# Performance work log

Hardware: AMD Instinct MI355X
Metric: run time of the kernel (lower is better)

Reference implementation:

```python
import jax, jax.numpy as jnp
import numpy as np

B, T, N, F_IN = 8, 12, 10000, 1
H = 32          # hidden_size
K = 2           # gnn_kernel (diffusion steps)
HORIZON = 12
E = 320000      # n_nodes * avg_degree 32


def setup_inputs() -> dict:
    key = jax.random.key(0)
    ks = jax.random.split(key, 12)
    s = 0.1  # weight scale to keep GRU in sane range
    return {
        "x": jax.random.normal(ks[0], (B, T, N, F_IN), jnp.float32),
        "edge_index": jax.random.randint(ks[1], (2, E), 0, N, dtype=jnp.int64),
        "edge_weight": jax.random.uniform(ks[2], (E,), jnp.float32),
        "enc_w": jax.random.normal(ks[3], (F_IN, H), jnp.float32) * s,
        "enc_b": jnp.zeros((H,), jnp.float32),
        "node_emb": jax.random.normal(ks[4], (N, H), jnp.float32) * s,
        "w_ih": jax.random.normal(ks[5], (3 * H, H), jnp.float32) * s,
        "w_hh": jax.random.normal(ks[6], (3 * H, H), jnp.float32) * s,
        "b_ih": jnp.zeros((3 * H,), jnp.float32),
        "b_hh": jnp.zeros((3 * H,), jnp.float32),
        "filt_w": jax.random.normal(ks[7], ((2 * K + 1) * H, H), jnp.float32) * s,
        "filt_b": jnp.zeros((H,), jnp.float32),
        "dec_w": jax.random.normal(ks[8], (H, F_IN * HORIZON), jnp.float32) * s,
        "dec_b": jnp.zeros((F_IN * HORIZON,), jnp.float32),
    }


def _gru_last(xs, w_ih, w_hh, b_ih, b_hh):
    # xs: [t, bn, H] -> last hidden state [bn, H]
    t, bn, h = xs.shape
    gx = jnp.einsum('tbh,gh->tbg', xs, w_ih) + b_ih  # [t, bn, 3H]

    def step(hid, gx_t):
        gh = hid @ w_hh.T + b_hh
        xr, xz, xn = jnp.split(gx_t, 3, axis=-1)
        hr, hz, hn = jnp.split(gh, 3, axis=-1)
        r = jax.nn.sigmoid(xr + hr)
        z = jax.nn.sigmoid(xz + hz)
        n_ = jnp.tanh(xn + r * hn)
        hid = (1.0 - z) * n_ + z * hid
        return hid, None

    h0 = jnp.zeros((bn, h), xs.dtype)
    h_last, _ = jax.lax.scan(step, h0, gx)
    return h_last


def _propagate(x, src, tgt, w, n):
    # x: [b, n, H]; out[:, tgt] += w * x[:, src]
    msgs = x[:, src, :] * w[None, :, None]  # [b, E, H]
    return jnp.zeros_like(x).at[:, tgt, :].add(msgs)


def reference(x, edge_index, edge_weight, enc_w, enc_b, node_emb,
              w_ih, w_hh, b_ih, b_hh, filt_w, filt_b, dec_w, dec_b):
    b, t, n, f_in = x.shape
    h = enc_w.shape[1]

    # ---- encoder + node embeddings ----
    x_enc = x @ enc_w + enc_b                       # [b, t, n, H]
    x_emb = x_enc + node_emb[None, None]            # broadcast add

    # ---- temporal GRU (per node, batch_first, last state) ----
    xs = jnp.transpose(x_emb, (1, 0, 2, 3)).reshape(t, b * n, h)
    h_time = _gru_last(xs, w_ih, w_hh, b_ih, b_hh).reshape(b, n, h)

    # ---- DiffConv: k-hop forward + backward diffusion ----
    src, tgt = edge_index[0], edge_index[1]
    deg_f = jnp.zeros((n,), edge_weight.dtype).at[tgt].add(edge_weight)
    w_f = edge_weight / jnp.where(deg_f[tgt] > 0, deg_f[tgt], 1.0)
    deg_b = jnp.zeros((n,), edge_weight.dtype).at[src].add(edge_weight)
    w_b = edge_weight / jnp.where(deg_b[src] > 0, deg_b[src], 1.0)

    outs = [h_time]  # root weight
    x_sup = h_time
    for _ in range(K):  # forward transition hops
        x_sup = _propagate(x_sup, src, tgt, w_f, n)
        outs.append(x_sup)
    x_sup = h_time
    for _ in range(K):  # backward (reversed edges) hops
        x_sup = _propagate(x_sup, tgt, src, w_b, n)
        outs.append(x_sup)
    z = jnp.concatenate(outs, axis=-1) @ filt_w + filt_b  # [b, n, H]

    # ---- decoder + rearrange 'b n (t f) -> b t n f' ----
    out = z @ dec_w + dec_b                                # [b, n, horizon*f_in]
    out = out.reshape(b, n, HORIZON, f_in)
    return jnp.transpose(out, (0, 2, 1, 3))                # [b, horizon, n, f_in]
```

## Files before the change

### kernel.cpp

```cpp
#include <hip/hip_runtime.h>
#include <hip/hip_fp16.h>

#define BB 8
#define TT 12
#define NN 10000
#define HH 32
#define EE 320000
#define HOR 12
#define NCB 157

static __device__ __forceinline__ float sigm(float x) {
    return __builtin_amdgcn_rcpf(1.0f + __expf(-x));
}
static __device__ __forceinline__ float tanh_fast(float x) {
    return 1.0f - 2.0f * __builtin_amdgcn_rcpf(1.0f + __expf(2.0f * x));
}
static __device__ __forceinline__ float2 uph2(unsigned u) {
    __half2 h = *(__half2*)&u;
    return __half22float2(h);
}
static __device__ __forceinline__ unsigned pkh2(float a, float b) {
    __half2 h = __floats2half2_rn(a, b);
    return *(unsigned*)&h;
}

typedef _Float16 f16x4 __attribute__((ext_vector_type(4)));
typedef float    f32x4 __attribute__((ext_vector_type(4)));

__global__ void k_zero(uint4* __restrict__ p, int n4) {
    int i = blockIdx.x * blockDim.x + threadIdx.x;
    if (i < n4) p[i] = (uint4){0u, 0u, 0u, 0u};
}

__global__ void k_cbhist(const float* __restrict__ node_emb, const float* __restrict__ enc_b,
                     const float* __restrict__ w_ih, const float* __restrict__ b_ih,
                     const float* __restrict__ b_hh,
                     const float* __restrict__ enc_w, const float* __restrict__ filt_w,
                     const float* __restrict__ filt_b, const float* __restrict__ dec_w,
                     const float* __restrict__ dec_b,
                     float* __restrict__ CB, float* __restrict__ A,
                     float* __restrict__ W2, float* __restrict__ b2,
                     const int* __restrict__ ei,
                     int* cnt_f, int* cnt_b,
                     int* __restrict__ rank_f, int* __restrict__ rank_b) {
    __shared__ float sw[96*36];
    __shared__ float semb[64*36];
    __shared__ float sbias[96];
    int bid = blockIdx.x;
    int tid = threadIdx.x;
    if (bid < NCB) {
        int n0 = bid * 64;
        for (int i = tid; i < 96*32; i += 256) {
            int g = i >> 5, h = i & 31;
            sw[g*36 + h] = w_ih[i];
        }
        for (int i = tid; i < 64*32; i += 256) {
            int row = i >> 5, h = i & 31;
            int n = n0 + row; if (n >= NN) n = NN-1;
            semb[row*36 + h] = enc_b[h] + node_emb[(size_t)n*32 + h];
        }
        if (tid < 96) sbias[tid] = b_ih[tid] + (tid < 64 ? b_hh[tid] : 0.f);
        __syncthreads();
        #pragma unroll 1
        for (int i = 0; i < 24; i++) {
            int o = i*256 + tid;
            int row = o / 96, g = o - row*96;
            int n = n0 + row;
            if (n < NN) {
                float s = sbias[g];
                const float4* ev = (const float4*)(semb + row*36);
                const float4* wv = (const float4*)(sw + g*36);
                #pragma unroll
                for (int q = 0; q < 8; q++) {
                    float4 e = ev[q], w = wv[q];
                    s = fmaf(e.x, w.x, s); s = fmaf(e.y, w.y, s);
                    s = fmaf(e.z, w.z, s); s = fmaf(e.w, w.w, s);
                }
                CB[(size_t)n*96 + g] = s;
            }
        }
    } else if (bid == NCB) {
        for (int i = tid; i < 96 + 160*12 + 12; i += blockDim.x) {
            if (i < 96) {
                float s = 0.f;
                for (int h = 0; h < HH; h++) s += enc_w[h] * w_ih[i*HH + h];
                A[i] = s;
            } else if (i < 96 + 1920) {
                int j = i - 96; int c = j / 12, o = j % 12;
                float s = 0.f;
                for (int h = 0; h < HH; h++) s += filt_w[c*HH + h] * dec_w[h*12 + o];
                W2[j] = s;
            } else {
                int o = i - 2016;
                float s = dec_b[o];
                for (int h = 0; h < HH; h++) s += filt_b[h] * dec_w[h*12 + o];
                b2[o] = s;
            }
        }
    } else {
        int e = (bid - NCB - 1) * 256 + tid;
        int s = ei[e], t = ei[EE + e];
        rank_f[e] = atomicAdd(&cnt_f[t], 1);
        rank_b[e] = atomicAdd(&cnt_b[s], 1);
    }
}

__global__ void k_scan(const int* __restrict__ cnt_f, int* off_f,
                       const int* __restrict__ cnt_b, int* off_b) {
    const int* cnt; int* off;
    if (blockIdx.x == 0) { cnt = cnt_f; off = off_f; }
    else                 { cnt = cnt_b; off = off_b; }
    __shared__ int part[1024];
    int t = threadIdx.x;
    const int CH = (NN + 1023) / 1024;
    int beg = t * CH, end = min(beg + CH, NN);
    int s = 0;
    for (int i = beg; i < end; i++) s += cnt[i];
    part[t] = s;
    __syncthreads();
    for (int d = 1; d < 1024; d <<= 1) {
        int add = (t >= d) ? part[t - d] : 0;
        __syncthreads();
        part[t] += add;
        __syncthreads();
    }
    int run = part[t] - s;
    for (int i = beg; i < end; i++) {
        off[i] = run; run += cnt[i];
    }
    if (t == 1023) off[NN] = part[1023];
}

__global__ __launch_bounds__(256) void k_grufill(const float* __restrict__ x,
                      const float* __restrict__ CB, const float* __restrict__ Ag,
                      const float* __restrict__ w_hh, const float* __restrict__ b_hh,
                      __half* __restrict__ hout16,
                      const int* __restrict__ ei, const float* __restrict__ ew,
                      const int* __restrict__ off_f, const int* __restrict__ rank_f,
                      unsigned long long* __restrict__ cfe,
                      const int* __restrict__ off_b, const int* __restrict__ rank_b,
                      unsigned long long* __restrict__ cbe) {
    int tid = threadIdx.x;
    if (blockIdx.x >= 1250) {
        int e = (blockIdx.x - 1250) * 256 + tid;
        int s = ei[e], t = ei[EE + e]; float w = ew[e];
        unsigned long long wb = (unsigned long long)__float_as_uint(w) << 32;
        cfe[off_f[t] + rank_f[e]] = wb | (unsigned)s;
        cbe[off_b[s] + rank_b[e]] = wb | (unsigned)t;
        return;
    }
    __shared__ unsigned sW[1536];
    __shared__ __half  shh[4][16*40];
    __shared__ float   sx[64][12];
    int r0b = blockIdx.x * 64;

    for (int d = tid; d < 1536; d += 256) {
        int fi = d >> 1, epair = d & 1;
        int l = fi & 63, tk = fi >> 6;
        int gt = tk >> 1, kh = tk & 1;
        int gate = 16*gt + (l & 15);
        int k = kh*16 + ((l >> 4) << 2) + 2*epair;
        sW[d] = pkh2(w_hh[gate*32 + k], w_hh[gate*32 + k + 1]);
    }
    for (int i = tid; i < 64*12; i += 256) {
        int row = i / 12, t = i - row*12;
        int r = r0b + row; int b = r / NN, n = r - b*NN;
        sx[row][t] = x[((size_t)b*TT + t)*NN + n];
    }
    __syncthreads();

    const int wv = tid >> 6, l = tid & 63;
    const int c = l & 15, m = l >> 4;
    const int r0w = r0b + wv*16;

    int bb[4], nn_[4];
    #pragma unroll
    for (int q = 0; q < 4; q++) {
        int r = r0w + 4*m + q;
        bb[q] = r / NN; nn_[q] = r - bb[q]*NN;
    }

    float cNx[2][4];
    f32x4 crv[2], czv[2], cnv[2];
    float aRj[2], aZj[2], aNj[2], bn0c[2];
    #pragma unroll
    for (int t2 = 0; t2 < 2; t2++) {
        int j = 16*t2 + c;
        #pragma unroll
        for (int q = 0; q < 4; q++) {
            const float* cb = CB + (size_t)nn_[q]*96;
            crv[t2][q] = cb[j];
            czv[t2][q] = cb[32 + j];
            cNx[t2][q] = cb[64 + j];
        }
        bn0c[t2] = b_hh[64 + j];
        cnv[t2] = (f32x4){bn0c[t2], bn0c[t2], bn0c[t2], bn0c[t2]};
        aRj[t2] = Ag[j]; aZj[t2] = Ag[32 + j]; aNj[t2] = Ag[64 + j];
    }

    f16x4 bf[12];
    #pragma unroll
    for (int i = 0; i < 12; i++) {
        unsigned long long v = *(const unsigned long long*)(sW + (i*64 + l)*2);
        bf[i] = __builtin_bit_cast(f16x4, v);
    }

    __half* hb = shh[wv];
    float own[2][4];
    {
        #pragma unroll
        for (int t2 = 0; t2 < 2; t2++)
        #pragma unroll
        for (int q = 0; q < 4; q++) {
            float xv = sx[wv*16 + 4*m + q][0];
            float rr = sigm(fmaf(xv, aRj[t2], crv[t2][q]));
            float zz = sigm(fmaf(xv, aZj[t2], czv[t2][q]));
            float nv = tanh_fast(fmaf(xv, aNj[t2], cNx[t2][q]) + rr * bn0c[t2]);
            own[t2][q] = (1.f - zz) * nv;
        }
    }
    #pragma unroll
    for (int t2 = 0; t2 < 2; t2++)
    #pragma unroll
    for (int q = 0; q < 4; q++)
        hb[(4*m + q)*40 + 16*t2 + c] = __float2half_rn(own[t2][q]);

    #pragma unroll 1
    for (int t = 1; t < TT; t++) {
        asm volatile("s_waitcnt lgkmcnt(0)" ::: "memory");
        __builtin_amdgcn_sched_barrier(0);
        unsigned long long va0 = *(const unsigned long long*)(hb + c*40 + m*4);
        unsigned long long va1 = *(const unsigned long long*)(hb + c*40 + 16 + m*4);
        f16x4 a0 = __builtin_bit_cast(f16x4, va0);
        f16x4 a1 = __builtin_bit_cast(f16x4, va1);
        float xq[4];
        #pragma unroll
        for (int q = 0; q < 4; q++) xq[q] = sx[wv*16 + 4*m + q][t];

        f32x4 aR[2], aZ[2], aN[2];
        #pragma unroll
        for (int t2 = 0; t2 < 2; t2++) {
            aR[t2] = __builtin_amdgcn_mfma_f32_16x16x16f16(a0, bf[(t2    )*2    ], crv[t2], 0, 0, 0);
            aR[t2] = __builtin_amdgcn_mfma_f32_16x16x16f16(a1, bf[(t2    )*2 + 1], aR[t2], 0, 0, 0);
            aZ[t2] = __builtin_amdgcn_mfma_f32_16x16x16f16(a0, bf[(2 + t2)*2    ], czv[t2], 0, 0, 0);
            aZ[t2] = __builtin_amdgcn_mfma_f32_16x16x16f16(a1, bf[(2 + t2)*2 + 1], aZ[t2], 0, 0, 0);
            aN[t2] = __builtin_amdgcn_mfma_f32_16x16x16f16(a0, bf[(4 + t2)*2    ], cnv[t2], 0, 0, 0);
            aN[t2] = __builtin_amdgcn_mfma_f32_16x16x16f16(a1, bf[(4 + t2)*2 + 1], aN[t2], 0, 0, 0);
        }
        #pragma unroll
        for (int t2 = 0; t2 < 2; t2++)
        #pragma unroll
        for (int q = 0; q < 4; q++) {
            float rr = sigm(fmaf(xq[q], aRj[t2], aR[t2][q]));
            float zz = sigm(fmaf(xq[q], aZj[t2], aZ[t2][q]));
            float nv = tanh_fast(fmaf(xq[q], aNj[t2], cNx[t2][q]) + rr * aN[t2][q]);
            own[t2][q] = (1.f - zz) * nv + zz * own[t2][q];
        }
        if (t < TT-1) {
            #pragma unroll
            for (int t2 = 0; t2 < 2; t2++)
            #pragma unroll
            for (int q = 0; q < 4; q++)
                hb[(4*m + q)*40 + 16*t2 + c] = __float2half_rn(own[t2][q]);
        }
    }
    #pragma unroll
    for (int t2 = 0; t2 < 2; t2++)
    #pragma unroll
    for (int q = 0; q < 4; q++)
        hout16[((size_t)nn_[q]*BB + bb[q])*HH + 16*t2 + c] = __float2half(own[t2][q]);
}

static __device__ __forceinline__ void gather_node(
        const unsigned* __restrict__ xu, const unsigned long long* __restrict__ ef,
        int e0, int e1, int l, float& a0, float& a1, float& a2, float& a3) {
    float ws = 0.f;
    a0 = a1 = a2 = a3 = 0.f;
    int e = e0;
    for (; e + 8 <= e1; e += 8) {
        unsigned long long q0 = ef[e],   q1 = ef[e+1], q2 = ef[e+2], q3 = ef[e+3];
        unsigned long long q4 = ef[e+4], q5 = ef[e+5], q6 = ef[e+6], q7 = ef[e+7];
        float w0 = __uint_as_float((unsigned)(q0 >> 32)), w1 = __uint_as_float((unsigned)(q1 >> 32));
        float w2 = __uint_as_float((unsigned)(q2 >> 32)), w3 = __uint_as_float((unsigned)(q3 >> 32));
        float w4 = __uint_as_float((unsigned)(q4 >> 32)), w5 = __uint_as_float((unsigned)(q5 >> 32));
        float w6 = __uint_as_float((unsigned)(q6 >> 32)), w7 = __uint_as_float((unsigned)(q7 >> 32));
        uint2 u0 = *(const uint2*)(xu + ((size_t)(unsigned)q0 << 7) + 2*l);
        uint2 u1 = *(const uint2*)(xu + ((size_t)(unsigned)q1 << 7) + 2*l);
        uint2 u2 = *(const uint2*)(xu + ((size_t)(unsigned)q2 << 7) + 2*l);
        uint2 u3 = *(const uint2*)(xu + ((size_t)(unsigned)q3 << 7) + 2*l);
        uint2 u4 = *(const uint2*)(xu + ((size_t)(unsigned)q4 << 7) + 2*l);
        uint2 u5 = *(const uint2*)(xu + ((size_t)(unsigned)q5 << 7) + 2*l);
        uint2 u6 = *(const uint2*)(xu + ((size_t)(unsigned)q6 << 7) + 2*l);
        uint2 u7 = *(const uint2*)(xu + ((size_t)(unsigned)q7 << 7) + 2*l);
        ws += ((w0 + w1) + (w2 + w3)) + ((w4 + w5) + (w6 + w7));
        float2 f;
        f = uph2(u0.x); a0 = fmaf(w0, f.x, a0); a1 = fmaf(w0, f.y, a1);
        f = uph2(u0.y); a2 = fmaf(w0, f.x, a2); a3 = fmaf(w0, f.y, a3);
        f = uph2(u1.x); a0 = fmaf(w1, f.x, a0); a1 = fmaf(w1, f.y, a1);
        f = uph2(u1.y); a2 = fmaf(w1, f.x, a2); a3 = fmaf(w1, f.y, a3);
        f = uph2(u2.x); a0 = fmaf(w2, f.x, a0); a1 = fmaf(w2, f.y, a1);
        f = uph2(u2.y); a2 = fmaf(w2, f.x, a2); a3 = fmaf(w2, f.y, a3);
        f = uph2(u3.x); a0 = fmaf(w3, f.x, a0); a1 = fmaf(w3, f.y, a1);
        f = uph2(u3.y); a2 = fmaf(w3, f.x, a2); a3 = fmaf(w3, f.y, a3);
        f = uph2(u4.x); a0 = fmaf(w4, f.x, a0); a1 = fmaf(w4, f.y, a1);
        f = uph2(u4.y); a2 = fmaf(w4, f.x, a2); a3 = fmaf(w4, f.y, a3);
        f = uph2(u5.x); a0 = fmaf(w5, f.x, a0); a1 = fmaf(w5, f.y, a1);
        f = uph2(u5.y); a2 = fmaf(w5, f.x, a2); a3 = fmaf(w5, f.y, a3);
        f = uph2(u6.x); a0 = fmaf(w6, f.x, a0); a1 = fmaf(w6, f.y, a1);
        f = uph2(u6.y); a2 = fmaf(w6, f.x, a2); a3 = fmaf(w6, f.y, a3);
        f = uph2(u7.x); a0 = fmaf(w7, f.x, a0); a1 = fmaf(w7, f.y, a1);
        f = uph2(u7.y); a2 = fmaf(w7, f.x, a2); a3 = fmaf(w7, f.y, a3);
    }
    for (; e < e1; ++e) {
        unsigned long long q0 = ef[e];
        float w0 = __uint_as_float((unsigned)(q0 >> 32));
        uint2 u0 = *(const uint2*)(xu + ((size_t)(unsigned)q0 << 7) + 2*l);
        ws += w0;
        float2 f;
        f = uph2(u0.x); a0 = fmaf(w0, f.x, a0); a1 = fmaf(w0, f.y, a1);
        f = uph2(u0.y); a2 = fmaf(w0, f.x, a2); a3 = fmaf(w0, f.y, a3);
    }
    float inv = ws > 0.f ? __builtin_amdgcn_rcpf(ws) : 1.0f;
    a0 *= inv; a1 *= inv; a2 *= inv; a3 *= inv;
}

__global__ __launch_bounds__(256) void k_prop(
        const __half* __restrict__ xF, const __half* __restrict__ xB,
        __half* __restrict__ yF16, __half* __restrict__ yB16,
        const int* __restrict__ offF, const unsigned long long* __restrict__ efF,
        const int* __restrict__ offB, const unsigned long long* __restrict__ efB) {
    int wid = threadIdx.x >> 6;
    int l   = threadIdx.x & 63;
    int nd = blockIdx.x * 4 + wid;
    int n = nd >> 1, dir = nd & 1;
    const unsigned* xu = (const unsigned*)(dir ? xB : xF);
    const int* off = dir ? offB : offF;
    const unsigned long long* ef = dir ? efB : efF;
    float a0, a1, a2, a3;
    gather_node(xu, ef, off[n], off[n+1], l, a0, a1, a2, a3);
    unsigned* yh = (unsigned*)(dir ? yB16 : yF16);
    uint2 oh; oh.x = pkh2(a0, a1); oh.y = pkh2(a2, a3);
    *(uint2*)(yh + ((size_t)n << 7) + 2*l) = oh;
}

__global__ __launch_bounds__(256) void k_prop2dec(
        const __half* __restrict__ aF, const __half* __restrict__ cBk,
        const __half* __restrict__ h16,
        const int* __restrict__ offF, const unsigned long long* __restrict__ efF,
        const int* __restrict__ offB, const unsigned long long* __restrict__ efB,
        const float* __restrict__ W2, const float* __restrict__ b2,
        float* __restrict__ out) {
    __shared__ float sW[1920];
    __shared__ float sb[12];
    __shared__ unsigned spc[4][2][128];
    int tid = threadIdx.x;
    for (int i = tid; i < 1920; i += 256) sW[i] = W2[i];
    if (tid < 12) sb[tid] = b2[tid];
    int wv = tid >> 6, l = tid & 63;
    int n = blockIdx.x * 4 + wv;
    {
        float a0, a1, a2, a3;
        gather_node((const unsigned*)aF, efF, offF[n], offF[n+1], l, a0, a1, a2, a3);
        spc[wv][0][2*l]   = pkh2(a0, a1);
        spc[wv][0][2*l+1] = pkh2(a2, a3);
    }
    {
        float a0, a1, a2, a3;
        gather_node((const unsigned*)cBk, efB, offB[n], offB[n+1], l, a0, a1, a2, a3);
        spc[wv][1][2*l]   = pkh2(a0, a1);
        spc[wv][1][2*l+1] = pkh2(a2, a3);
    }
    __syncthreads();
    if (tid < 128) {
        int nl = tid >> 5;
        int b  = (tid >> 2) & 7;
        int tq = tid & 3;
        int node = blockIdx.x * 4 + nl;
        size_t base = ((size_t)node * BB + b) * HH;
        float a[3];
        #pragma unroll
        for (int o = 0; o < 3; o++) a[o] = sb[3*tq + o];
        const __half* gp[3] = {h16, aF, cBk};
        const int wo[3] = {0, 32, 96};
        #pragma unroll
        for (int gi = 0; gi < 3; gi++) {
            const uint4* pp = (const uint4*)(gp[gi] + base);
            const float* wbase = sW + wo[gi]*12 + 3*tq;
            #pragma unroll
            for (int q = 0; q < 4; q++) {
                uint4 v = pp[q];
                float2 f0 = uph2(v.x), f1 = uph2(v.y), f2 = uph2(v.z), f3 = uph2(v.w);
                float pv[8] = {f0.x, f0.y, f1.x, f1.y, f2.x, f2.y, f3.x, f3.y};
                #pragma unroll
                for (int k = 0; k < 8; k++) {
                    const float* wrow = wbase + (q*8 + k)*12;
                    #pragma unroll
                    for (int o = 0; o < 3; o++) a[o] = fmaf(pv[k], wrow[o], a[o]);
                }
            }
        }
        #pragma unroll
        for (int dir = 0; dir < 2; dir++) {
            const uint4* pp = (const uint4*)&spc[nl][dir][b*16];
            const float* wbase = sW + (64 + dir*64)*12 + 3*tq;
            #pragma unroll
            for (int q = 0; q < 4; q++) {
                uint4 v = pp[q];
                float2 f0 = uph2(v.x), f1 = uph2(v.y), f2 = uph2(v.z), f3 = uph2(v.w);
                float pv[8] = {f0.x, f0.y, f1.x, f1.y, f2.x, f2.y, f3.x, f3.y};
                #pragma unroll
                for (int k = 0; k < 8; k++) {
                    const float* wrow = wbase + (q*8 + k)*12;
                    #pragma unroll
                    for (int o = 0; o < 3; o++) a[o] = fmaf(pv[k], wrow[o], a[o]);
                }
            }
        }
        #pragma unroll
        for (int o = 0; o < 3; o++)
            out[((size_t)(b*HOR + 3*tq + o))*NN + node] = a[o];
    }
}

extern "C" void kernel_launch(void* const* d_in, const int* in_sizes, int n_in,
                              void* d_out, int out_size, void* d_ws, size_t ws_size,
                              hipStream_t stream) {
    const float* x      = (const float*)d_in[0];
    const int*   ei     = (const int*)d_in[1];
    const float* ew     = (const float*)d_in[2];
    const float* enc_w  = (const float*)d_in[3];
    const float* enc_b  = (const float*)d_in[4];
    const float* nemb   = (const float*)d_in[5];
    const float* w_ih   = (const float*)d_in[6];
    const float* w_hh   = (const float*)d_in[7];
    const float* b_ih   = (const float*)d_in[8];
    const float* b_hh   = (const float*)d_in[9];
    const float* filt_w = (const float*)d_in[10];
    const float* filt_b = (const float*)d_in[11];
    const float* dec_w  = (const float*)d_in[12];
    const float* dec_b  = (const float*)d_in[13];
    float* out = (float*)d_out;

    char* p = (char*)d_ws;
    auto alloc = [&](size_t bytes) -> char* {
        char* q = p; p += (bytes + 255) & ~(size_t)255; return q;
    };
    char* zero_base = p;
    int*   cnt_f = (int*)  alloc((size_t)NN*4);
    int*   cnt_b = (int*)  alloc((size_t)NN*4);
    size_t zero_bytes = (size_t)(p - zero_base);
    int zero_n4 = (int)(zero_bytes / 16);

    const size_t SROW = (size_t)BB*NN*HH;
    __half* h16    = (__half*)alloc(SROW*2);
    __half* a16    = (__half*)alloc(SROW*2);
    __half* c16    = (__half*)alloc(SROW*2);
    float* CB     = (float*)alloc((size_t)NN*96*4);
    float* A      = (float*)alloc(96*4);
    float* W2     = (float*)alloc(1920*4);
    float* b2     = (float*)alloc(12*4);
    int*   off_f  = (int*)  alloc((size_t)(NN+1)*4);
    int*   off_b  = (int*)  alloc((size_t)(NN+1)*4);
    int*   rank_f = (int*)  alloc((size_t)EE*4);
    int*   rank_b = (int*)  alloc((size_t)EE*4);
    unsigned long long* cfe = (unsigned long long*)alloc((size_t)EE*8);
    unsigned long long* cbe = (unsigned long long*)alloc((size_t)EE*8);

    k_zero<<<(zero_n4 + 255)/256, 256, 0, stream>>>((uint4*)zero_base, zero_n4);

    k_cbhist<<<NCB + 1 + EE/256, 256, 0, stream>>>(nemb, enc_b, w_ih, b_ih, b_hh,
                                       enc_w, filt_w, filt_b, dec_w, dec_b,
                                       CB, A, W2, b2, ei, cnt_f, cnt_b,
                                       rank_f, rank_b);
    k_scan<<<2, 1024, 0, stream>>>(cnt_f, off_f, cnt_b, off_b);

    k_grufill<<<2500, 256, 0, stream>>>(x, CB, A, w_hh, b_hh, h16,
                                        ei, ew, off_f, rank_f, cfe,
                                        off_b, rank_b, cbe);

    k_prop<<<5000, 256, 0, stream>>>(h16, h16, a16, c16,
                                     off_f, cfe, off_b, cbe);
    k_prop2dec<<<2500, 256, 0, stream>>>(a16, c16, h16,
                                         off_f, cfe, off_b, cbe,
                                         W2, b2, out);
}
```

Baseline: 182.0 us.

## Split hidden states into batch-pair slices for cache-local graph gathers

Hidden-state storage changes from [node][batch][H] to four slices of [batch-pair][node][64 halves]. The propagation kernels now gather per slice with 128-byte rows, two edge groups per wave reduced by a shuffle, and nontemporal edge loads. Block indexing interleaves the slices so that each working set of gathered rows is smaller and more likely to stay in cache. In exchange the grid is four times larger, the edge lists are reread once per slice, and the decoder work uses fewer threads.

```diff
diff --git a/kernel.cpp b/kernel.cpp
--- a/kernel.cpp
+++ b/kernel.cpp
@@ -8,6 +8,8 @@
 #define EE 320000
 #define HOR 12
 #define NCB 157
+
+typedef unsigned long long ull;
 
 static __device__ __forceinline__ float sigm(float x) {
     return __builtin_amdgcn_rcpf(1.0f + __expf(-x));
@@ -137,14 +139,14 @@
                       __half* __restrict__ hout16,
                       const int* __restrict__ ei, const float* __restrict__ ew,
                       const int* __restrict__ off_f, const int* __restrict__ rank_f,
-                      unsigned long long* __restrict__ cfe,
+                      ull* __restrict__ cfe,
                       const int* __restrict__ off_b, const int* __restrict__ rank_b,
-                      unsigned long long* __restrict__ cbe) {
+                      ull* __restrict__ cbe) {
     int tid = threadIdx.x;
     if (blockIdx.x >= 1250) {
         int e = (blockIdx.x - 1250) * 256 + tid;
         int s = ei[e], t = ei[EE + e]; float w = ew[e];
-        unsigned long long wb = (unsigned long long)__float_as_uint(w) << 32;
+        ull wb = (ull)__float_as_uint(w) << 32;
         cfe[off_f[t] + rank_f[e]] = wb | (unsigned)s;
         cbe[off_b[s] + rank_b[e]] = wb | (unsigned)t;
         return;
@@ -201,7 +203,7 @@
     f16x4 bf[12];
     #pragma unroll
     for (int i = 0; i < 12; i++) {
-        unsigned long long v = *(const unsigned long long*)(sW + (i*64 + l)*2);
+        ull v = *(const ull*)(sW + (i*64 + l)*2);
         bf[i] = __builtin_bit_cast(f16x4, v);
     }
 
@@ -229,8 +231,8 @@
     for (int t = 1; t < TT; t++) {
         asm volatile("s_waitcnt lgkmcnt(0)" ::: "memory");
         __builtin_amdgcn_sched_barrier(0);
-        unsigned long long va0 = *(const unsigned long long*)(hb + c*40 + m*4);
-        unsigned long long va1 = *(const unsigned long long*)(hb + c*40 + 16 + m*4);
+        ull va0 = *(const ull*)(hb + c*40 + m*4);
+        ull va1 = *(const ull*)(hb + c*40 + 16 + m*4);
         f16x4 a0 = __builtin_bit_cast(f16x4, va0);
         f16x4 a1 = __builtin_bit_cast(f16x4, va1);
         float xq[4];
@@ -267,158 +269,135 @@
     #pragma unroll
     for (int t2 = 0; t2 < 2; t2++)
     #pragma unroll
-    for (int q = 0; q < 4; q++)
-        hout16[((size_t)nn_[q]*BB + bb[q])*HH + 16*t2 + c] = __float2half(own[t2][q]);
-}
-
-static __device__ __forceinline__ void gather_node(
-        const unsigned* __restrict__ xu, const unsigned long long* __restrict__ ef,
-        int e0, int e1, int l, float& a0, float& a1, float& a2, float& a3) {
+    for (int q = 0; q < 4; q++) {
+        size_t idx = ((size_t)((bb[q] >> 1)*NN + nn_[q]) << 6)
+                   + ((bb[q] & 1) << 5) + 16*t2 + c;
+        hout16[idx] = __float2half(own[t2][q]);
+    }
+}
+
+static __device__ __forceinline__ void gather_slice(
+        const unsigned* __restrict__ xu, unsigned rowbase ,
+        const ull* __restrict__ ef, int e0, int e1, int eg, int sub,
+        float& a0, float& a1) {
     float ws = 0.f;
-    a0 = a1 = a2 = a3 = 0.f;
-    int e = e0;
-    for (; e + 8 <= e1; e += 8) {
-        unsigned long long q0 = ef[e],   q1 = ef[e+1], q2 = ef[e+2], q3 = ef[e+3];
-        unsigned long long q4 = ef[e+4], q5 = ef[e+5], q6 = ef[e+6], q7 = ef[e+7];
-        float w0 = __uint_as_float((unsigned)(q0 >> 32)), w1 = __uint_as_float((unsigned)(q1 >> 32));
-        float w2 = __uint_as_float((unsigned)(q2 >> 32)), w3 = __uint_as_float((unsigned)(q3 >> 32));
-        float w4 = __uint_as_float((unsigned)(q4 >> 32)), w5 = __uint_as_float((unsigned)(q5 >> 32));
-        float w6 = __uint_as_float((unsigned)(q6 >> 32)), w7 = __uint_as_float((unsigned)(q7 >> 32));
-        uint2 u0 = *(const uint2*)(xu + ((size_t)(unsigned)q0 << 7) + 2*l);
-        uint2 u1 = *(const uint2*)(xu + ((size_t)(unsigned)q1 << 7) + 2*l);
-        uint2 u2 = *(const uint2*)(xu + ((size_t)(unsigned)q2 << 7) + 2*l);
-        uint2 u3 = *(const uint2*)(xu + ((size_t)(unsigned)q3 << 7) + 2*l);
-        uint2 u4 = *(const uint2*)(xu + ((size_t)(unsigned)q4 << 7) + 2*l);
-        uint2 u5 = *(const uint2*)(xu + ((size_t)(unsigned)q5 << 7) + 2*l);
-        uint2 u6 = *(const uint2*)(xu + ((size_t)(unsigned)q6 << 7) + 2*l);
-        uint2 u7 = *(const uint2*)(xu + ((size_t)(unsigned)q7 << 7) + 2*l);
-        ws += ((w0 + w1) + (w2 + w3)) + ((w4 + w5) + (w6 + w7));
+    a0 = 0.f; a1 = 0.f;
+    for (int e = e0; e < e1; e += 8) {
+        int ee0 = e + eg, ee1 = e + 2 + eg, ee2 = e + 4 + eg, ee3 = e + 6 + eg;
+        ull q0 = ee0 < e1 ? __builtin_nontemporal_load(ef + ee0) : 0ULL;
+        ull q1 = ee1 < e1 ? __builtin_nontemporal_load(ef + ee1) : 0ULL;
+        ull q2 = ee2 < e1 ? __builtin_nontemporal_load(ef + ee2) : 0ULL;
+        ull q3 = ee3 < e1 ? __builtin_nontemporal_load(ef + ee3) : 0ULL;
+        float w0 = __uint_as_float((unsigned)(q0 >> 32));
+        float w1 = __uint_as_float((unsigned)(q1 >> 32));
+        float w2 = __uint_as_float((unsigned)(q2 >> 32));
+        float w3 = __uint_as_float((unsigned)(q3 >> 32));
+        unsigned u0 = xu[((size_t)(rowbase + (unsigned)q0) << 5) + sub];
+        unsigned u1 = xu[((size_t)(rowbase + (unsigned)q1) << 5) + sub];
+        unsigned u2 = xu[((size_t)(rowbase + (unsigned)q2) << 5) + sub];
+        unsigned u3 = xu[((size_t)(rowbase + (unsigned)q3) << 5) + sub];
+        ws += (w0 + w1) + (w2 + w3);
         float2 f;
-        f = uph2(u0.x); a0 = fmaf(w0, f.x, a0); a1 = fmaf(w0, f.y, a1);
-        f = uph2(u0.y); a2 = fmaf(w0, f.x, a2); a3 = fmaf(w0, f.y, a3);
-        f = uph2(u1.x); a0 = fmaf(w1, f.x, a0); a1 = fmaf(w1, f.y, a1);
-        f = uph2(u1.y); a2 = fmaf(w1, f.x, a2); a3 = fmaf(w1, f.y, a3);
-        f = uph2(u2.x); a0 = fmaf(w2, f.x, a0); a1 = fmaf(w2, f.y, a1);
-        f = uph2(u2.y); a2 = fmaf(w2, f.x, a2); a3 = fmaf(w2, f.y, a3);
-        f = uph2(u3.x); a0 = fmaf(w3, f.x, a0); a1 = fmaf(w3, f.y, a1);
-        f = uph2(u3.y); a2 = fmaf(w3, f.x, a2); a3 = fmaf(w3, f.y, a3);
-        f = uph2(u4.x); a0 = fmaf(w4, f.x, a0); a1 = fmaf(w4, f.y, a1);
-        f = uph2(u4.y); a2 = fmaf(w4, f.x, a2); a3 = fmaf(w4, f.y, a3);
-        f = uph2(u5.x); a0 = fmaf(w5, f.x, a0); a1 = fmaf(w5, f.y, a1);
-        f = uph2(u5.y); a2 = fmaf(w5, f.x, a2); a3 = fmaf(w5, f.y, a3);
-        f = uph2(u6.x); a0 = fmaf(w6, f.x, a0); a1 = fmaf(w6, f.y, a1);
-        f = uph2(u6.y); a2 = fmaf(w6, f.x, a2); a3 = fmaf(w6, f.y, a3);
-        f = uph2(u7.x); a0 = fmaf(w7, f.x, a0); a1 = fmaf(w7, f.y, a1);
-        f = uph2(u7.y); a2 = fmaf(w7, f.x, a2); a3 = fmaf(w7, f.y, a3);
-    }
-    for (; e < e1; ++e) {
-        unsigned long long q0 = ef[e];
-        float w0 = __uint_as_float((unsigned)(q0 >> 32));
-        uint2 u0 = *(const uint2*)(xu + ((size_t)(unsigned)q0 << 7) + 2*l);
-        ws += w0;
-        float2 f;
-        f = uph2(u0.x); a0 = fmaf(w0, f.x, a0); a1 = fmaf(w0, f.y, a1);
-        f = uph2(u0.y); a2 = fmaf(w0, f.x, a2); a3 = fmaf(w0, f.y, a3);
-    }
+        f = uph2(u0); a0 = fmaf(w0, f.x, a0); a1 = fmaf(w0, f.y, a1);
+        f = uph2(u1); a0 = fmaf(w1, f.x, a0); a1 = fmaf(w1, f.y, a1);
+        f = uph2(u2); a0 = fmaf(w2, f.x, a0); a1 = fmaf(w2, f.y, a1);
+        f = uph2(u3); a0 = fmaf(w3, f.x, a0); a1 = fmaf(w3, f.y, a1);
+    }
+    a0 += __shfl_xor(a0, 32);
+    a1 += __shfl_xor(a1, 32);
+    ws += __shfl_xor(ws, 32);
     float inv = ws > 0.f ? __builtin_amdgcn_rcpf(ws) : 1.0f;
-    a0 *= inv; a1 *= inv; a2 *= inv; a3 *= inv;
+    a0 *= inv; a1 *= inv;
 }
 
 __global__ __launch_bounds__(256) void k_prop(
-        const __half* __restrict__ xF, const __half* __restrict__ xB,
-        __half* __restrict__ yF16, __half* __restrict__ yB16,
-        const int* __restrict__ offF, const unsigned long long* __restrict__ efF,
-        const int* __restrict__ offB, const unsigned long long* __restrict__ efB) {
-    int wid = threadIdx.x >> 6;
-    int l   = threadIdx.x & 63;
-    int nd = blockIdx.x * 4 + wid;
-    int n = nd >> 1, dir = nd & 1;
-    const unsigned* xu = (const unsigned*)(dir ? xB : xF);
+        const __half* __restrict__ h16,
+        __half* __restrict__ a16, __half* __restrict__ c16,
+        const int* __restrict__ offF, const ull* __restrict__ efF,
+        const int* __restrict__ offB, const ull* __restrict__ efB) {
+    int bid = blockIdx.x;
+    int s = (bid & 7) >> 1;
+    int inner = (bid >> 3) * 2 + (bid & 1);
+    int wid = threadIdx.x >> 6, l = threadIdx.x & 63;
+    int node = inner*2 + (wid >> 1), dir = wid & 1;
+    int eg = l >> 5, sub = l & 31;
+    unsigned rowbase = (unsigned)(s * NN);
     const int* off = dir ? offB : offF;
-    const unsigned long long* ef = dir ? efB : efF;
-    float a0, a1, a2, a3;
-    gather_node(xu, ef, off[n], off[n+1], l, a0, a1, a2, a3);
-    unsigned* yh = (unsigned*)(dir ? yB16 : yF16);
-    uint2 oh; oh.x = pkh2(a0, a1); oh.y = pkh2(a2, a3);
-    *(uint2*)(yh + ((size_t)n << 7) + 2*l) = oh;
+    const ull* ef = dir ? efB : efF;
+    float a0, a1;
+    gather_slice((const unsigned*)h16, rowbase, ef, off[node], off[node+1],
+                 eg, sub, a0, a1);
+    if (l < 32) {
+        unsigned* y = (unsigned*)(dir ? c16 : a16);
+        y[((size_t)(rowbase + node) << 5) + l] = pkh2(a0, a1);
+    }
 }
 
 __global__ __launch_bounds__(256) void k_prop2dec(
         const __half* __restrict__ aF, const __half* __restrict__ cBk,
         const __half* __restrict__ h16,
-        const int* __restrict__ offF, const unsigned long long* __restrict__ efF,
-        const int* __restrict__ offB, const unsigned long long* __restrict__ efB,
+        const int* __restrict__ offF, const ull* __restrict__ efF,
+        const int* __restrict__ offB, const ull* __restrict__ efB,
         const float* __restrict__ W2, const float* __restrict__ b2,
         float* __restrict__ out) {
     __shared__ float sW[1920];
     __shared__ float sb[12];
-    __shared__ unsigned spc[4][2][128];
+    __shared__ unsigned spc[4][32];
     int tid = threadIdx.x;
     for (int i = tid; i < 1920; i += 256) sW[i] = W2[i];
     if (tid < 12) sb[tid] = b2[tid];
-    int wv = tid >> 6, l = tid & 63;
-    int n = blockIdx.x * 4 + wv;
+    int bid = blockIdx.x;
+    int s = (bid & 7) >> 1;
+    int inner = (bid >> 3) * 2 + (bid & 1);
+    int node0 = inner * 2;
+    int wid = tid >> 6, l = tid & 63;
+    int node = node0 + (wid >> 1), dir = wid & 1;
+    int eg = l >> 5, sub = l & 31;
+    unsigned rowbase = (unsigned)(s * NN);
     {
-        float a0, a1, a2, a3;
-        gather_node((const unsigned*)aF, efF, offF[n], offF[n+1], l, a0, a1, a2, a3);
-        spc[wv][0][2*l]   = pkh2(a0, a1);
-        spc[wv][0][2*l+1] = pkh2(a2, a3);
-    }
-    {
-        float a0, a1, a2, a3;
-        gather_node((const unsigned*)cBk, efB, offB[n], offB[n+1], l, a0, a1, a2, a3);
-        spc[wv][1][2*l]   = pkh2(a0, a1);
-        spc[wv][1][2*l+1] = pkh2(a2, a3);
+        const __half* src = dir ? cBk : aF;
+        const int* off = dir ? offB : offF;
+        const ull* ef = dir ? efB : efF;
+        float a0, a1;
+        gather_slice((const unsigned*)src, rowbase, ef, off[node], off[node+1],
+                     eg, sub, a0, a1);
+        if (l < 32) spc[wid][sub] = pkh2(a0, a1);
     }
     __syncthreads();
-    if (tid < 128) {
-        int nl = tid >> 5;
-        int b  = (tid >> 2) & 7;
-        int tq = tid & 3;
-        int node = blockIdx.x * 4 + nl;
-        size_t base = ((size_t)node * BB + b) * HH;
-        float a[3];
-        #pragma unroll
-        for (int o = 0; o < 3; o++) a[o] = sb[3*tq + o];
-        const __half* gp[3] = {h16, aF, cBk};
+    if (tid < 48) {
+        int p = tid / 12;
+        int o = tid - p*12;
+        int nl = p >> 1, bl = p & 1;
+        int nd = node0 + nl;
+        int b = 2*s + bl;
+        float acc = sb[o];
+        size_t dbase = ((size_t)(rowbase + nd) << 5) + (bl << 4);
+        const unsigned* gp[3] = {(const unsigned*)h16 + dbase,
+                                 (const unsigned*)aF + dbase,
+                                 (const unsigned*)cBk + dbase};
         const int wo[3] = {0, 32, 96};
         #pragma unroll
         for (int gi = 0; gi < 3; gi++) {
-            const uint4* pp = (const uint4*)(gp[gi] + base);
-            const float* wbase = sW + wo[gi]*12 + 3*tq;
+            const unsigned* pp = gp[gi];
             #pragma unroll
-            for (int q = 0; q < 4; q++) {
-                uint4 v = pp[q];
-                float2 f0 = uph2(v.x), f1 = uph2(v.y), f2 = uph2(v.z), f3 = uph2(v.w);
-                float pv[8] = {f0.x, f0.y, f1.x, f1.y, f2.x, f2.y, f3.x, f3.y};
-                #pragma unroll
-                for (int k = 0; k < 8; k++) {
-                    const float* wrow = wbase + (q*8 + k)*12;
-                    #pragma unroll
-                    for (int o = 0; o < 3; o++) a[o] = fmaf(pv[k], wrow[o], a[o]);
-                }
+            for (int d = 0; d < 16; d++) {
+                float2 f = uph2(pp[d]);
+                acc = fmaf(f.x, sW[(wo[gi] + 2*d    )*12 + o], acc);
+                acc = fmaf(f.y, sW[(wo[gi] + 2*d + 1)*12 + o], acc);
             }
         }
         #pragma unroll
-        for (int dir = 0; dir < 2; dir++) {
-            const uint4* pp = (const uint4*)&spc[nl][dir][b*16];
-            const float* wbase = sW + (64 + dir*64)*12 + 3*tq;
+        for (int dd = 0; dd < 2; dd++) {
+            const unsigned* pp = &spc[nl*2 + dd][bl << 4];
+            int wbase = 64 + dd*64;
             #pragma unroll
-            for (int q = 0; q < 4; q++) {
-                uint4 v = pp[q];
-                float2 f0 = uph2(v.x), f1 = uph2(v.y), f2 = uph2(v.z), f3 = uph2(v.w);
-                float pv[8] = {f0.x, f0.y, f1.x, f1.y, f2.x, f2.y, f3.x, f3.y};
-                #pragma unroll
-                for (int k = 0; k < 8; k++) {
-                    const float* wrow = wbase + (q*8 + k)*12;
-                    #pragma unroll
-                    for (int o = 0; o < 3; o++) a[o] = fmaf(pv[k], wrow[o], a[o]);
-                }
+            for (int d = 0; d < 16; d++) {
+                float2 f = uph2(pp[d]);
+                acc = fmaf(f.x, sW[(wbase + 2*d    )*12 + o], acc);
+                acc = fmaf(f.y, sW[(wbase + 2*d + 1)*12 + o], acc);
             }
         }
-        #pragma unroll
-        for (int o = 0; o < 3; o++)
-            out[((size_t)(b*HOR + 3*tq + o))*NN + node] = a[o];
+        out[((size_t)(b*HOR + o))*NN + nd] = acc;
     }
 }
 
@@ -463,8 +442,8 @@
     int*   off_b  = (int*)  alloc((size_t)(NN+1)*4);
     int*   rank_f = (int*)  alloc((size_t)EE*4);
     int*   rank_b = (int*)  alloc((size_t)EE*4);
-    unsigned long long* cfe = (unsigned long long*)alloc((size_t)EE*8);
-    unsigned long long* cbe = (unsigned long long*)alloc((size_t)EE*8);
+    ull*   cfe    = (ull*)  alloc((size_t)EE*8);
+    ull*   cbe    = (ull*)  alloc((size_t)EE*8);
 
     k_zero<<<(zero_n4 + 255)/256, 256, 0, stream>>>((uint4*)zero_base, zero_n4);
 
@@ -478,9 +457,9 @@
                                         ei, ew, off_f, rank_f, cfe,
                                         off_b, rank_b, cbe);
 
-    k_prop<<<5000, 256, 0, stream>>>(h16, h16, a16, c16,
-                                     off_f, cfe, off_b, cbe);
-    k_prop2dec<<<2500, 256, 0, stream>>>(a16, c16, h16,
-                                         off_f, cfe, off_b, cbe,
-                                         W2, b2, out);
-}
+    k_prop<<<20000, 256, 0, stream>>>(h16, a16, c16,
+                                      off_f, cfe, off_b, cbe);
+    k_prop2dec<<<20000, 256, 0, stream>>>(a16, c16, h16,
+                                          off_f, cfe, off_b, cbe,
+                                          W2, b2, out);
+}
```

New measurement: 278.4 us. +53.0%, slower.
